# Performance work log

Measured on AMD Instinct MI355X. Metric: run time of the kernel, lower is better.

## Reference

```python
import jax, jax.numpy as jnp
import numpy as np

N, B, T = 2048, 16, 256

def setup_inputs() -> dict:
    key = jax.random.key(0)
    k1, k2, k3, k4 = jax.random.split(key, 4)
    x = jax.random.normal(k1, (B, T, N), dtype=jnp.float32)
    weight = jax.random.normal(k2, (T, T), dtype=jnp.float32) * (1.0 / np.sqrt(T))
    bias = jax.random.normal(k3, (T,), dtype=jnp.float32) * 0.01
    # Gumbel(0,1) noise, matching torch.nn.functional.gumbel_softmax internals
    u = jax.random.uniform(k4, (N * N, 2), dtype=jnp.float32, minval=1e-6, maxval=1.0 - 1e-6)
    gumbel = -jnp.log(-jnp.log(u))
    return {"x": x, "weight": weight, "bias": bias, "gumbel": gumbel}

def reference(x, weight, bias, gumbel):
    # x: [B, T, N] -> node-major [N, B, T]
    xp = jnp.transpose(x, (2, 0, 1))
    n = xp.shape[0]
    # --- similarity-based logits (torch writes via .data -> no grad path) ---
    xs = jax.lax.stop_gradient(xp)
    x_avg = xs.mean(axis=1)                                          # [N, T]
    x_norm = x_avg / jnp.maximum(jnp.linalg.norm(x_avg, axis=-1, keepdims=True), 1e-12)
    sim = (x_norm @ x_norm.T + 1.0) * 0.5                            # [N, N] in [0,1]
    sim_flat = sim.reshape(-1)
    # gumbel_softmax(hard=True) forward: adjacency = argmax over (logits + g)
    score0 = sim_flat + gumbel[:, 0]
    score1 = (1.0 - sim_flat) + gumbel[:, 1]
    adj = (score0 > score1).astype(xp.dtype).reshape(n, n)           # directed adjacency
    # --- structural coefficient (dense, faithful to compute_structural_coeff) ---
    adj_sym = jnp.clip(adj + adj.T, 0.0, 1.0)
    nmask = jnp.clip(adj_sym + jnp.eye(n, dtype=xp.dtype), 0.0, 1.0)
    common = nmask @ nmask.T                                         # common-neighbor counts
    max_common = common.max()                                        # >= 1 (diagonal)
    valid = (adj_sym * (common > 1.0).astype(xp.dtype)) > 0
    struct = jnp.where(valid, (common / max_common) * common, 0.0)   # lambda_val = 1.0
    # edge weights only at directed-edge positions
    W = adj * struct                                                 # [src, dst]
    # --- gcn_norm (no self loops, improved=False): deg over dst, D^-1/2 W D^-1/2 ---
    deg = W.sum(axis=0)
    dinv = jnp.where(deg > 0, deg ** -0.5, 0.0)
    Wn = dinv[:, None] * W * dinv[None, :]
    # --- linear + gather-multiply-scatter aggregation (out[d] = sum_s Wn[s,d] x[s]) ---
    xw = jnp.einsum('nbt,to->nbo', xp, weight)                       # [N, B, T]
    out = jnp.einsum('sd,sbt->dbt', Wn, xw) + bias                   # [N, B, T]
    return jnp.transpose(out, (1, 2, 0))                             # [B, T, N]
```

## Files before the change

### kernel.cpp

```cpp
#include <hip/hip_runtime.h>

#define NN 2048
#define BB 16
#define TT 256

typedef unsigned short ushort_t;
typedef unsigned char u8;
typedef short bf16x8 __attribute__((ext_vector_type(8)));
typedef float f32x4 __attribute__((ext_vector_type(4)));
typedef int i32x4 __attribute__((ext_vector_type(4)));

__device__ __forceinline__ ushort_t f2bf(float f) {
    unsigned u = __float_as_uint(f);
    return (ushort_t)((u + 0x7FFFu + ((u >> 16) & 1u)) >> 16);
}

__device__ __forceinline__ void gload16(const void* g, void* l) {
    __builtin_amdgcn_global_load_lds((const __attribute__((address_space(1))) unsigned int*)g,
                                     (__attribute__((address_space(3))) unsigned int*)l,
                                     16, 0, 0);
}

#define SBAR() asm volatile("s_barrier" ::: "memory")

__device__ __forceinline__ void mfma3_bf16_128(
    const ushort_t* __restrict__ Ag, size_t lda,
    const ushort_t* __restrict__ Bg, size_t ldb,
    int m0, int n0, int nkt,
    ushort_t (*As)[128][32], ushort_t (*Bs)[128][32],
    f32x4 (&acc)[4][4], int tid)
{
    const int lane = tid & 63, wave = tid >> 6;
    const int wr = wave >> 1, wc = wave & 1;
    const int r0 = tid >> 2, kc = (tid & 3) * 8;
    const int lr = lane & 15, kg = (lane >> 4) * 8;
#define STAGE_BF(kt, buf) { \
        const int k0_ = (kt) * 32; \
        gload16(&Ag[(size_t)(m0 + r0) * lda + k0_ + kc], &As[buf][r0][kc]); \
        gload16(&Ag[(size_t)(m0 + r0 + 64) * lda + k0_ + kc], &As[buf][r0 + 64][kc]); \
        gload16(&Bg[(size_t)(n0 + r0) * ldb + k0_ + kc], &Bs[buf][r0][kc]); \
        gload16(&Bg[(size_t)(n0 + r0 + 64) * ldb + k0_ + kc], &Bs[buf][r0 + 64][kc]); \
    }
    STAGE_BF(0, 0);
    STAGE_BF(1, 1);
    for (int kt = 0; kt < nkt; kt++) {
        if (kt + 1 < nkt) asm volatile("s_waitcnt vmcnt(4)" ::: "memory");
        else              asm volatile("s_waitcnt vmcnt(0)" ::: "memory");
        SBAR();
        if (kt + 2 < nkt) STAGE_BF(kt + 2, (kt + 2) % 3);
        const int cur = kt % 3;
        bf16x8 af[4], bfj[4];
#pragma unroll
        for (int f = 0; f < 4; f++) {
            af[f]  = *(const bf16x8*)&As[cur][wr * 64 + f * 16 + lr][kg];
            bfj[f] = *(const bf16x8*)&Bs[cur][wc * 64 + f * 16 + lr][kg];
        }
#pragma unroll
        for (int i = 0; i < 4; i++)
#pragma unroll
            for (int j = 0; j < 4; j++)
                acc[i][j] = __builtin_amdgcn_mfma_f32_16x16x32_bf16(af[i], bfj[j], acc[i][j], 0, 0, 0);
    }
#undef STAGE_BF
}

__device__ __forceinline__ void mfma3_i8_128x64(
    const u8* __restrict__ Ag, size_t lda,
    const u8* __restrict__ Bg, size_t ldb,
    int m0, int n0, int nkt,
    u8 (*As)[128][64], u8 (*Bs)[64][64],
    i32x4 (&acc)[4][2], int tid)
{
    const int lane = tid & 63, wave = tid >> 6;
    const int wr = wave >> 1, wc = wave & 1;
    const int r0 = tid >> 2, kc = (tid & 3) * 16;
    const int lr = lane & 15, kg = (lane >> 4) * 16;
#define STAGE_I8(kt, buf) { \
        const int k0_ = (kt) * 64; \
        gload16(&Ag[(size_t)(m0 + r0) * lda + k0_ + kc], &As[buf][r0][kc]); \
        gload16(&Ag[(size_t)(m0 + r0 + 64) * lda + k0_ + kc], &As[buf][r0 + 64][kc]); \
        gload16(&Bg[(size_t)(n0 + r0) * ldb + k0_ + kc], &Bs[buf][r0][kc]); \
    }
    STAGE_I8(0, 0);
    STAGE_I8(1, 1);
    for (int kt = 0; kt < nkt; kt++) {
        if (kt + 1 < nkt) asm volatile("s_waitcnt vmcnt(3)" ::: "memory");
        else              asm volatile("s_waitcnt vmcnt(0)" ::: "memory");
        SBAR();
        if (kt + 2 < nkt) STAGE_I8(kt + 2, (kt + 2) % 3);
        const int cur = kt % 3;
        i32x4 af[4], bfj[2];
#pragma unroll
        for (int f = 0; f < 4; f++) af[f] = *(const i32x4*)&As[cur][wr * 64 + f * 16 + lr][kg];
#pragma unroll
        for (int j = 0; j < 2; j++) bfj[j] = *(const i32x4*)&Bs[cur][wc * 32 + j * 16 + lr][kg];
#pragma unroll
        for (int i = 0; i < 4; i++)
#pragma unroll
            for (int j = 0; j < 2; j++)
                acc[i][j] = __builtin_amdgcn_mfma_i32_16x16x64_i8(af[i], bfj[j], acc[i][j], 0, 0, 0);
    }
#undef STAGE_I8
}

__global__ __launch_bounds__(256) void k_xts(const float* __restrict__ x,
                                             ushort_t* __restrict__ xT,
                                             float* __restrict__ xsumT,
                                             float* __restrict__ ssq) {
    __shared__ float tile[32][33];
    __shared__ float ssqp[32];
    const int n0 = blockIdx.x * 32, t0 = blockIdx.y * 32;
    const int tid = threadIdx.x;
    const int r = tid >> 3, c4 = (tid & 7) * 4;
    if (tid < 32) ssqp[tid] = 0.f;
    float4 acc = {0.f, 0.f, 0.f, 0.f};
    for (int b = 0; b < BB; b++) {
        const float4 v = *(const float4*)&x[(size_t)((b * TT) + t0 + r) * NN + n0 + c4];
        acc.x += v.x; acc.y += v.y; acc.z += v.z; acc.w += v.w;
        __syncthreads();
        tile[r][c4 + 0] = v.x; tile[r][c4 + 1] = v.y;
        tile[r][c4 + 2] = v.z; tile[r][c4 + 3] = v.w;
        __syncthreads();
        ushort4 o;
        o.x = f2bf(tile[c4 + 0][r]); o.y = f2bf(tile[c4 + 1][r]);
        o.z = f2bf(tile[c4 + 2][r]); o.w = f2bf(tile[c4 + 3][r]);
        *(ushort4*)&xT[(size_t)(b * NN + n0 + r) * TT + t0 + c4] = o;
    }
    *(float4*)&xsumT[(size_t)(t0 + r) * NN + n0 + c4] = acc;
    atomicAdd(&ssqp[c4 + 0], acc.x * acc.x);
    atomicAdd(&ssqp[c4 + 1], acc.y * acc.y);
    atomicAdd(&ssqp[c4 + 2], acc.z * acc.z);
    atomicAdd(&ssqp[c4 + 3], acc.w * acc.w);
    __syncthreads();
    if (tid < 32) atomicAdd(&ssq[n0 + tid], ssqp[tid]);
}

__global__ __launch_bounds__(256) void k_adj(const float* __restrict__ A,
                                             const float* __restrict__ ssq,
                                             const float* __restrict__ gumbel,
                                             u8* __restrict__ adjb) {
    __shared__ __align__(16) float As[2][32][64];
    __shared__ __align__(16) float Bs[2][32][64];
    const int m0 = blockIdx.y * 64, n0 = blockIdx.x * 64;
    const int tid = threadIdx.x;
    const int tx = tid & 15, ty = tid >> 4;
    const int sr = tid >> 4, sc = (tid & 15) * 4;
    float acc[4][4];
#pragma unroll
    for (int i = 0; i < 4; i++)
#pragma unroll
        for (int j = 0; j < 4; j++) acc[i][j] = 0.f;
    gload16(&A[(size_t)sr * NN + m0 + sc], &As[0][sr][sc]);
    gload16(&A[(size_t)sr * NN + n0 + sc], &Bs[0][sr][sc]);
    gload16(&A[(size_t)(sr + 16) * NN + m0 + sc], &As[0][sr + 16][sc]);
    gload16(&A[(size_t)(sr + 16) * NN + n0 + sc], &Bs[0][sr + 16][sc]);
    __syncthreads();
    int cur = 0;
    for (int kt = 0; kt < 8; kt++) {
        if (kt + 1 < 8) {
            const int k0 = (kt + 1) * 32;
            gload16(&A[(size_t)(k0 + sr) * NN + m0 + sc], &As[cur ^ 1][sr][sc]);
            gload16(&A[(size_t)(k0 + sr) * NN + n0 + sc], &Bs[cur ^ 1][sr][sc]);
            gload16(&A[(size_t)(k0 + sr + 16) * NN + m0 + sc], &As[cur ^ 1][sr + 16][sc]);
            gload16(&A[(size_t)(k0 + sr + 16) * NN + n0 + sc], &Bs[cur ^ 1][sr + 16][sc]);
        }
#pragma unroll 16
        for (int kk = 0; kk < 32; kk++) {
            float4 a = *(const float4*)&As[cur][kk][ty * 4];
            float4 b = *(const float4*)&Bs[cur][kk][tx * 4];
            const float av[4] = {a.x, a.y, a.z, a.w};
            const float bv[4] = {b.x, b.y, b.z, b.w};
#pragma unroll
            for (int i = 0; i < 4; i++)
#pragma unroll
                for (int j = 0; j < 4; j++) acc[i][j] = fmaf(av[i], bv[j], acc[i][j]);
        }
        __syncthreads();
        cur ^= 1;
    }
    float invi[4], invj[4];
#pragma unroll
    for (int i = 0; i < 4; i++) {
        const float si = ssq[m0 + ty * 4 + i];
        invi[i] = (si > 0.f) ? rsqrtf(si) : 0.f;
        const float sj = ssq[n0 + tx * 4 + i];
        invj[i] = (sj > 0.f) ? rsqrtf(sj) : 0.f;
    }
#pragma unroll
    for (int i = 0; i < 4; i++) {
        const int gi = m0 + ty * 4 + i;
        const size_t rowb = (size_t)gi * NN + n0 + tx * 4;
#pragma unroll
        for (int j = 0; j < 4; j++) {
            const float dot = acc[i][j] * invi[i] * invj[j];
            const float2 g = *(const float2*)&gumbel[2 * (rowb + j)];
            adjb[rowb + j] = (dot > g.y - g.x) ? (u8)1 : (u8)0;
        }
    }
}

__global__ __launch_bounds__(256) void k_nmask(const u8* __restrict__ adjb,
                                               u8* __restrict__ nm) {
    __shared__ u8 tt[32][33];
    const int J = blockIdx.x * 32, I = blockIdx.y * 32;
    const int c = threadIdx.x & 31, r0 = threadIdx.x >> 5;
#pragma unroll
    for (int r = r0; r < 32; r += 8) tt[r][c] = adjb[(size_t)(J + r) * NN + I + c];
    __syncthreads();
#pragma unroll
    for (int r = r0; r < 32; r += 8) {
        const int gi = I + r, gj = J + c;
        const bool on = (gi == gj) || adjb[(size_t)gi * NN + gj] || tt[c][r];
        nm[(size_t)gi * NN + gj] = on ? (u8)1 : (u8)0;
    }
}

__global__ __launch_bounds__(256) void k_commonW(const u8* __restrict__ nm,
                                                 const u8* __restrict__ adjb,
                                                 float* __restrict__ W,
                                                 float* __restrict__ deg) {
    __shared__ __align__(16) u8 As[3][128][64];
    __shared__ __align__(16) u8 Bs[3][64][64];
    const int m0 = blockIdx.y * 128, n0 = blockIdx.x * 64;
    const int tid = threadIdx.x;
    const int lane = tid & 63, wave = tid >> 6;
    const int wr = wave >> 1, wc = wave & 1;
    i32x4 acc[4][2];
#pragma unroll
    for (int i = 0; i < 4; i++)
#pragma unroll
        for (int j = 0; j < 2; j++) acc[i][j] = (i32x4){0, 0, 0, 0};
    mfma3_i8_128x64(nm, NN, nm, NN, m0, n0, NN / 64, As, Bs, acc, tid);
    const int lr = lane & 15, rg = (lane >> 4) * 4;
#pragma unroll
    for (int j = 0; j < 2; j++) {
        const int gj = n0 + wc * 32 + j * 16 + lr;
        float psum = 0.f;
#pragma unroll
        for (int i = 0; i < 4; i++)
#pragma unroll
            for (int r = 0; r < 4; r++) {
                const int gi = m0 + wr * 64 + i * 16 + rg + r;
                const int cv = acc[i][j][r];
                const size_t fl = (size_t)gi * NN + gj;
                const float cf = (float)cv;
                const float wv = (cv > 1 && adjb[fl]) ? cf * cf : 0.f;
                W[fl] = wv;
                psum += wv;
            }
        atomicAdd(&deg[gj], psum);
    }
}

__global__ __launch_bounds__(256) void k_wtn(const float* __restrict__ W,
                                             const float* __restrict__ deg,
                                             ushort_t* __restrict__ Wtn) {
    __shared__ float tt[64][65];
    const int S0 = blockIdx.x * 64, D0 = blockIdx.y * 64;
    const int c = threadIdx.x & 63, r0 = threadIdx.x >> 6;
#pragma unroll
    for (int r = r0; r < 64; r += 4) tt[r][c] = W[(size_t)(S0 + r) * NN + D0 + c];
    __syncthreads();
    const float dgs = deg[S0 + c];
    const float ds = (dgs > 0.f) ? rsqrtf(dgs) : 0.f;
#pragma unroll
    for (int r = r0; r < 64; r += 4) {
        const int d = D0 + r;
        const float dgd = deg[d];
        const float dd = (dgd > 0.f) ? rsqrtf(dgd) : 0.f;
        Wtn[(size_t)d * NN + S0 + c] = f2bf(tt[c][r] * ds * dd);
    }
}

__global__ __launch_bounds__(256) void k_wt(const float* __restrict__ w,
                                            ushort_t* __restrict__ wT) {
    __shared__ float tile[64][65];
    const int t0 = blockIdx.y * 64, o0 = blockIdx.x * 64;
    const int c = threadIdx.x & 63, r0 = threadIdx.x >> 6;
#pragma unroll
    for (int r = r0; r < 64; r += 4)
        tile[r][c] = w[(size_t)(t0 + r) * TT + o0 + c];
    __syncthreads();
#pragma unroll
    for (int r = r0; r < 64; r += 4)
        wT[(size_t)(o0 + r) * TT + t0 + c] = f2bf(tile[c][r]);
}

__global__ __launch_bounds__(256) void k_xw(const ushort_t* __restrict__ wT,
                                            const ushort_t* __restrict__ xT,
                                            ushort_t* __restrict__ xwT) {
    __shared__ __align__(16) ushort_t As[3][128][32];
    __shared__ __align__(16) ushort_t Bs[3][128][32];
    const int b = blockIdx.z;
    const ushort_t* __restrict__ Bg = xT + (size_t)b * NN * TT;
    const int m0 = blockIdx.y * 128, n0 = blockIdx.x * 128;
    const int tid = threadIdx.x;
    const int lane = tid & 63, wave = tid >> 6;
    const int wr = wave >> 1, wc = wave & 1;
    f32x4 acc[4][4];
#pragma unroll
    for (int i = 0; i < 4; i++)
#pragma unroll
        for (int j = 0; j < 4; j++) acc[i][j] = (f32x4){0.f, 0.f, 0.f, 0.f};
    mfma3_bf16_128(wT, TT, Bg, TT, m0, n0, TT / 32, As, Bs, acc, tid);
    const int lr = lane & 15, rg = (lane >> 4) * 4;
#pragma unroll
    for (int i = 0; i < 4; i++)
#pragma unroll
        for (int j = 0; j < 4; j++)
#pragma unroll
            for (int r = 0; r < 4; r++) {
                const int o = m0 + wr * 64 + i * 16 + rg + r;
                const int n = n0 + wc * 64 + j * 16 + lr;
                xwT[((size_t)b * TT + o) * NN + n] = f2bf(acc[i][j][r]);
            }
}

__global__ __launch_bounds__(256) void k_out(const ushort_t* __restrict__ xwT,
                                             const ushort_t* __restrict__ Wtn,
                                             const float* __restrict__ bias,
                                             float* __restrict__ out) {
    __shared__ __align__(16) ushort_t As[3][128][32];
    __shared__ __align__(16) ushort_t Bs[3][128][32];
    const int m0 = blockIdx.y * 128, n0 = blockIdx.x * 128;
    const int tid = threadIdx.x;
    const int lane = tid & 63, wave = tid >> 6;
    const int wr = wave >> 1, wc = wave & 1;
    f32x4 acc[4][4];
#pragma unroll
    for (int i = 0; i < 4; i++)
#pragma unroll
        for (int j = 0; j < 4; j++) acc[i][j] = (f32x4){0.f, 0.f, 0.f, 0.f};
    mfma3_bf16_128(xwT, NN, Wtn, NN, m0, n0, NN / 32, As, Bs, acc, tid);
    const int lr = lane & 15, rg = (lane >> 4) * 4;
#pragma unroll
    for (int i = 0; i < 4; i++)
#pragma unroll
        for (int j = 0; j < 4; j++)
#pragma unroll
            for (int r = 0; r < 4; r++) {
                const int gm = m0 + wr * 64 + i * 16 + rg + r;
                const int gd = n0 + wc * 64 + j * 16 + lr;
                out[(size_t)gm * NN + gd] = acc[i][j][r] + bias[gm & (TT - 1)];
            }
}

extern "C" void kernel_launch(void* const* d_in, const int* in_sizes, int n_in,
                              void* d_out, int out_size, void* d_ws, size_t ws_size,
                              hipStream_t stream) {
    const float* x      = (const float*)d_in[0];
    const float* w      = (const float*)d_in[1];
    const float* bias   = (const float*)d_in[2];
    const float* gumbel = (const float*)d_in[3];
    float* out = (float*)d_out;

    char* ws = (char*)d_ws;
    float*    xsumT = (float*)(ws + 0);
    float*    ssq   = (float*)(ws + 2097152);
    float*    deg   = (float*)(ws + 2105344);
    u8*       adjb  = (u8*)(ws + 2113536);
    u8*       nm    = (u8*)(ws + 6307840);
    float*    W     = (float*)(ws + 10502144);
    ushort_t* xwT   = (ushort_t*)(ws + 10502144);
    ushort_t* Wtn   = (ushort_t*)(ws + 27279360);
    ushort_t* xT    = (ushort_t*)(ws + 35667968);
    ushort_t* wT    = (ushort_t*)(ws + 52445184);

    hipMemsetAsync(ws + 2097152, 0, 16384, stream);

    k_xts    <<<dim3(NN / 32, TT / 32), 256, 0, stream>>>(x, xT, xsumT, ssq);
    k_adj    <<<dim3(32, 32),           256, 0, stream>>>(xsumT, ssq, gumbel, adjb);
    k_nmask  <<<dim3(64, 64),           256, 0, stream>>>(adjb, nm);
    k_commonW<<<dim3(NN / 64, NN / 128),256, 0, stream>>>(nm, adjb, W, deg);
    k_wtn    <<<dim3(32, 32),           256, 0, stream>>>(W, deg, Wtn);
    k_wt     <<<dim3(4, 4),             256, 0, stream>>>(w, wT);
    k_xw     <<<dim3(NN / 128, TT / 128, BB),   256, 0, stream>>>(wT, xT, xwT);
    k_out    <<<dim3(NN / 128, (BB * TT) / 128), 256, 0, stream>>>(xwT, Wtn, bias, out);
}
```

Before: 275.6 us.

## Deepen GEMM LDS pipeline to four stages and add XCD-aware block swizzle

```diff
diff --git a/kernel.cpp b/kernel.cpp
--- a/kernel.cpp
+++ b/kernel.cpp
@@ -23,7 +23,7 @@
 
 #define SBAR() asm volatile("s_barrier" ::: "memory")
 
-__device__ __forceinline__ void mfma3_bf16_128(
+__device__ __forceinline__ void mfma4_bf16_128(
     const ushort_t* __restrict__ Ag, size_t lda,
     const ushort_t* __restrict__ Bg, size_t ldb,
     int m0, int n0, int nkt,
@@ -41,14 +41,15 @@
         gload16(&Bg[(size_t)(n0 + r0) * ldb + k0_ + kc], &Bs[buf][r0][kc]); \
         gload16(&Bg[(size_t)(n0 + r0 + 64) * ldb + k0_ + kc], &Bs[buf][r0 + 64][kc]); \
     }
-    STAGE_BF(0, 0);
-    STAGE_BF(1, 1);
+    for (int p = 0; p < 3 && p < nkt; p++) STAGE_BF(p, p);
     for (int kt = 0; kt < nkt; kt++) {
-        if (kt + 1 < nkt) asm volatile("s_waitcnt vmcnt(4)" ::: "memory");
-        else              asm volatile("s_waitcnt vmcnt(0)" ::: "memory");
+        const int rem = nkt - 1 - kt;
+        if (rem >= 2)      asm volatile("s_waitcnt vmcnt(8)" ::: "memory");
+        else if (rem == 1) asm volatile("s_waitcnt vmcnt(4)" ::: "memory");
+        else               asm volatile("s_waitcnt vmcnt(0)" ::: "memory");
         SBAR();
-        if (kt + 2 < nkt) STAGE_BF(kt + 2, (kt + 2) % 3);
-        const int cur = kt % 3;
+        if (kt + 3 < nkt) STAGE_BF(kt + 3, (kt + 3) & 3);
+        const int cur = kt & 3;
         bf16x8 af[4], bfj[4];
 #pragma unroll
         for (int f = 0; f < 4; f++) {
@@ -64,7 +65,7 @@
 #undef STAGE_BF
 }
 
-__device__ __forceinline__ void mfma3_i8_128x64(
+__device__ __forceinline__ void mfma4_i8_128x64(
     const u8* __restrict__ Ag, size_t lda,
     const u8* __restrict__ Bg, size_t ldb,
     int m0, int n0, int nkt,
@@ -81,14 +82,15 @@
         gload16(&Ag[(size_t)(m0 + r0 + 64) * lda + k0_ + kc], &As[buf][r0 + 64][kc]); \
         gload16(&Bg[(size_t)(n0 + r0) * ldb + k0_ + kc], &Bs[buf][r0][kc]); \
     }
-    STAGE_I8(0, 0);
-    STAGE_I8(1, 1);
+    for (int p = 0; p < 3 && p < nkt; p++) STAGE_I8(p, p);
     for (int kt = 0; kt < nkt; kt++) {
-        if (kt + 1 < nkt) asm volatile("s_waitcnt vmcnt(3)" ::: "memory");
-        else              asm volatile("s_waitcnt vmcnt(0)" ::: "memory");
+        const int rem = nkt - 1 - kt;
+        if (rem >= 2)      asm volatile("s_waitcnt vmcnt(6)" ::: "memory");
+        else if (rem == 1) asm volatile("s_waitcnt vmcnt(3)" ::: "memory");
+        else               asm volatile("s_waitcnt vmcnt(0)" ::: "memory");
         SBAR();
-        if (kt + 2 < nkt) STAGE_I8(kt + 2, (kt + 2) % 3);
-        const int cur = kt % 3;
+        if (kt + 3 < nkt) STAGE_I8(kt + 3, (kt + 3) & 3);
+        const int cur = kt & 3;
         i32x4 af[4], bfj[2];
 #pragma unroll
         for (int f = 0; f < 4; f++) af[f] = *(const i32x4*)&As[cur][wr * 64 + f * 16 + lr][kg];
@@ -219,9 +221,13 @@
                                                  const u8* __restrict__ adjb,
                                                  float* __restrict__ W,
                                                  float* __restrict__ deg) {
-    __shared__ __align__(16) u8 As[3][128][64];
-    __shared__ __align__(16) u8 Bs[3][64][64];
-    const int m0 = blockIdx.y * 128, n0 = blockIdx.x * 64;
+    __shared__ __align__(16) u8 As[4][128][64];
+    __shared__ __align__(16) u8 Bs[4][64][64];
+    const int id = blockIdx.y * 32 + blockIdx.x;
+    const int xcd = id & 7, c = id >> 3;
+    const int bx = ((xcd & 1) << 4) | (c & 15);
+    const int by = ((xcd >> 1) << 2) | (c >> 4);
+    const int m0 = by * 128, n0 = bx * 64;
     const int tid = threadIdx.x;
     const int lane = tid & 63, wave = tid >> 6;
     const int wr = wave >> 1, wc = wave & 1;
@@ -230,7 +236,7 @@
     for (int i = 0; i < 4; i++)
 #pragma unroll
         for (int j = 0; j < 2; j++) acc[i][j] = (i32x4){0, 0, 0, 0};
-    mfma3_i8_128x64(nm, NN, nm, NN, m0, n0, NN / 64, As, Bs, acc, tid);
+    mfma4_i8_128x64(nm, NN, nm, NN, m0, n0, NN / 64, As, Bs, acc, tid);
     const int lr = lane & 15, rg = (lane >> 4) * 4;
 #pragma unroll
     for (int j = 0; j < 2; j++) {
@@ -289,8 +295,8 @@
 __global__ __launch_bounds__(256) void k_xw(const ushort_t* __restrict__ wT,
                                             const ushort_t* __restrict__ xT,
                                             ushort_t* __restrict__ xwT) {
-    __shared__ __align__(16) ushort_t As[3][128][32];
-    __shared__ __align__(16) ushort_t Bs[3][128][32];
+    __shared__ __align__(16) ushort_t As[4][128][32];
+    __shared__ __align__(16) ushort_t Bs[4][128][32];
     const int b = blockIdx.z;
     const ushort_t* __restrict__ Bg = xT + (size_t)b * NN * TT;
     const int m0 = blockIdx.y * 128, n0 = blockIdx.x * 128;
@@ -302,7 +308,7 @@
     for (int i = 0; i < 4; i++)
 #pragma unroll
         for (int j = 0; j < 4; j++) acc[i][j] = (f32x4){0.f, 0.f, 0.f, 0.f};
-    mfma3_bf16_128(wT, TT, Bg, TT, m0, n0, TT / 32, As, Bs, acc, tid);
+    mfma4_bf16_128(wT, TT, Bg, TT, m0, n0, TT / 32, As, Bs, acc, tid);
     const int lr = lane & 15, rg = (lane >> 4) * 4;
 #pragma unroll
     for (int i = 0; i < 4; i++)
@@ -320,9 +326,13 @@
                                              const ushort_t* __restrict__ Wtn,
                                              const float* __restrict__ bias,
                                              float* __restrict__ out) {
-    __shared__ __align__(16) ushort_t As[3][128][32];
-    __shared__ __align__(16) ushort_t Bs[3][128][32];
-    const int m0 = blockIdx.y * 128, n0 = blockIdx.x * 128;
+    __shared__ __align__(16) ushort_t As[4][128][32];
+    __shared__ __align__(16) ushort_t Bs[4][128][32];
+    const int id = blockIdx.y * 16 + blockIdx.x;
+    const int xcd = id & 7, c = id >> 3;
+    const int bx = ((xcd & 1) << 3) | (c & 7);
+    const int by = ((xcd >> 1) << 3) | (c >> 3);
+    const int m0 = by * 128, n0 = bx * 128;
     const int tid = threadIdx.x;
     const int lane = tid & 63, wave = tid >> 6;
     const int wr = wave >> 1, wc = wave & 1;
@@ -331,7 +341,7 @@
     for (int i = 0; i < 4; i++)
 #pragma unroll
         for (int j = 0; j < 4; j++) acc[i][j] = (f32x4){0.f, 0.f, 0.f, 0.f};
-    mfma3_bf16_128(xwT, NN, Wtn, NN, m0, n0, NN / 32, As, Bs, acc, tid);
+    mfma4_bf16_128(xwT, NN, Wtn, NN, m0, n0, NN / 32, As, Bs, acc, tid);
     const int lr = lane & 15, rg = (lane >> 4) * 4;
 #pragma unroll
     for (int i = 0; i < 4; i++)
```

Measured after the change: 270.2 us. 2.0% less time.
